# Optimization experiments

Hardware: AMD Instinct MI355X
Metric: run time of the kernel (lower is better)

## Reference

```python
import jax, jax.numpy as jnp
import numpy as np
import math

EMBED_DIM = 2048
NUM_HEADS = 32
GROUPS = 4
HEAD_DIM = EMBED_DIM // NUM_HEADS  # 64
HPG = NUM_HEADS // GROUPS          # heads per group = 8


def setup_inputs() -> dict:
    key = jax.random.key(0)
    k_x, k_wq, k_bq, k_wkv, k_bkv = jax.random.split(key, 5)
    B, L = 4, 4096
    scale = 1.0 / math.sqrt(EMBED_DIM)
    return {
        "x": jax.random.normal(k_x, (B, L, EMBED_DIM), dtype=jnp.float32),
        "Wq": jax.random.normal(k_wq, (EMBED_DIM, EMBED_DIM), dtype=jnp.float32) * scale,
        "bq": jax.random.normal(k_bq, (EMBED_DIM,), dtype=jnp.float32) * 0.01,
        "Wkv": jax.random.normal(k_wkv, (EMBED_DIM, 2 * HEAD_DIM * GROUPS), dtype=jnp.float32) * scale,
        "bkv": jax.random.normal(k_bkv, (2 * HEAD_DIM * GROUPS,), dtype=jnp.float32) * 0.01,
    }


def reference(x, Wq, bq, Wkv, bkv):
    B, L, _ = x.shape
    # projections
    q = (x @ Wq + bq).reshape(B, L, GROUPS, HPG, HEAD_DIM)          # blghd
    kv = (x @ Wkv + bkv).reshape(B, L, GROUPS, 2, HEAD_DIM)
    k, v = kv[:, :, :, 0], kv[:, :, :, 1]                            # blgd
    # scores: q @ k^T with k of shape (..., 1, head_dim) -> (..., HPG, 1)
    scores = jnp.einsum("blghd,blgd->blgh", q, k)[..., None] / math.sqrt(HEAD_DIM)
    attn = jax.nn.softmax(scores, axis=-1)                           # size-1 axis -> ones
    # attn @ v: (..., HPG, 1) @ (..., 1, head_dim) -> (..., HPG, head_dim)
    out = attn * v[:, :, :, None, :]                                 # blghd
    return out.reshape(B, L, EMBED_DIM)
```

## Files before the change

kernel.cpp:

```cpp
#include <hip/hip_runtime.h>


#define EMBED 2048
#define SV 272

typedef _Float16 half8 __attribute__((ext_vector_type(8)));
typedef _Float16 half4v __attribute__((ext_vector_type(4)));
typedef float f32x4 __attribute__((ext_vector_type(4)));

#define GLOAD16(g, l)                                                      \
  __builtin_amdgcn_global_load_lds(                                        \
      (const __attribute__((address_space(1))) void*)(g),                  \
      (__attribute__((address_space(3))) void*)(l), 16, 0, 0)

__global__ __launch_bounds__(256) void prep_b(const float* __restrict__ Wkv,
                                              _Float16* __restrict__ Bt) {
  const int t = threadIdx.x;
  const int kb = blockIdx.x * 4;
  const int vcol = ((t >> 6) * 128) + 64 + (t & 63);
  float v[4];
#pragma unroll
  for (int i = 0; i < 4; ++i) v[i] = Wkv[(size_t)(kb + i) * 512 + vcol];
  half4v h;
#pragma unroll
  for (int i = 0; i < 4; ++i) h[i] = (_Float16)v[i];
  *(half4v*)&Bt[(size_t)t * EMBED + kb] = h;
}

__global__ __launch_bounds__(256) void gqa_main(
    const float* __restrict__ x, const _Float16* __restrict__ Bt,
    const float* __restrict__ bkv, float* __restrict__ out) {
  __shared__ __align__(16) char smem[3 * 16384 + 3 * 32768];
  char* const Ab = smem;
  char* const Bb = smem + 3 * 16384;
  float* const Vs = (float*)smem;

  const int tid = threadIdx.x;
  const int w = tid >> 6;
  const int lane = tid & 63;
  const int lm = lane & 15;
  const int lq = lane >> 4;
  const int row0 = blockIdx.x * 64;

  const int acol = ((lane & 7) ^ (lane >> 3)) << 4;
  const char* asrc = (const char*)x +
      (size_t)(row0 + w * 16 + (lane >> 3)) * (EMBED * 4) + acol;
  const int adst0 = (w * 16) * 128;
  const int bcol = (((lane & 3) ^ ((lane >> 3) & 3)) << 4);
  const char* bsrc = (const char*)Bt +
      (size_t)(w * 64 + (lane >> 2)) * (EMBED * 2) + bcol;
  const int bdst0 = (w * 64) * 64;

#define STAGE(b, s)                                                        \
  {                                                                        \
    const char* as_ = asrc + (size_t)(s) * 256;                            \
    char* ad_ = Ab + (b) * 16384 + adst0;                                  \
    GLOAD16(as_, ad_);                                                     \
    GLOAD16(as_ + (size_t)8 * EMBED * 4, ad_ + 1024);                      \
    GLOAD16(as_ + 128, ad_ + 8192);                                        \
    GLOAD16(as_ + (size_t)8 * EMBED * 4 + 128, ad_ + 8192 + 1024);         \
    const char* bs_ = bsrc + (size_t)(s) * 128;                            \
    char* bd_ = Bb + (b) * 32768 + bdst0;                                  \
    GLOAD16(bs_, bd_);                                                     \
    GLOAD16(bs_ + (size_t)16 * EMBED * 2, bd_ + 1024);                     \
    GLOAD16(bs_ + (size_t)32 * EMBED * 2, bd_ + 2048);                     \
    GLOAD16(bs_ + (size_t)48 * EMBED * 2, bd_ + 3072);                     \
    GLOAD16(bs_ + 64, bd_ + 16384);                                        \
    GLOAD16(bs_ + (size_t)16 * EMBED * 2 + 64, bd_ + 16384 + 1024);        \
    GLOAD16(bs_ + (size_t)32 * EMBED * 2 + 64, bd_ + 16384 + 2048);        \
    GLOAD16(bs_ + (size_t)48 * EMBED * 2 + 64, bd_ + 16384 + 3072);        \
  }

  const int arswz = (lm & 7) << 4;
  const int brswz = ((lm >> 1) & 3) << 4;

#define LOADFRAG(b, roa, rob)                                              \
  {                                                                        \
    const char* Ar_ = Ab + (b) * 16384 + (roa) + lm * 128;                 \
    const char* Br_ = Bb + (b) * 32768 + (rob) + (w * 64 + lm) * 64 +      \
                      ((lq << 4) ^ brswz);                                 \
    _Pragma("unroll") for (int ni = 0; ni < 4; ++ni)                       \
        bfr_[ni] = *(const half8*)(Br_ + ni * 1024);                       \
    _Pragma("unroll") for (int mi = 0; mi < 4; ++mi) {                     \
      a0r_[mi] = *(const f32x4*)(Ar_ + mi * 2048 + ((lq << 5) ^ arswz));   \
      a1r_[mi] =                                                           \
          *(const f32x4*)(Ar_ + mi * 2048 + (((lq << 5) + 16) ^ arswz));   \
    }                                                                      \
  }
#define MFMAFRAG()                                                         \
  _Pragma("unroll") for (int mi = 0; mi < 4; ++mi) {                       \
    half8 af_;                                                             \
    _Pragma("unroll") for (int j = 0; j < 4; ++j)                          \
        af_[j] = (_Float16)a0r_[mi][j];                                    \
    _Pragma("unroll") for (int j = 0; j < 4; ++j)                          \
        af_[4 + j] = (_Float16)a1r_[mi][j];                                \
    _Pragma("unroll") for (int ni = 0; ni < 4; ++ni)                       \
        acc[mi][ni] = __builtin_amdgcn_mfma_f32_16x16x32_f16(              \
            af_, bfr_[ni], acc[mi][ni], 0, 0, 0);                          \
  }

  f32x4 acc[4][4] = {};

  STAGE(0, 0);
  STAGE(1, 1);

#define ITER(T, BC, BS)                                                    \
  {                                                                        \
    asm volatile("s_waitcnt vmcnt(12)" ::: "memory");                      \
    __builtin_amdgcn_s_barrier();                                          \
    f32x4 a0r_[4], a1r_[4];                                                \
    half8 bfr_[4];                                                         \
    LOADFRAG(BC, 0, 0);                                                    \
    {                                                                      \
      const int ss_ = (T) + 2 < 32 ? (T) + 2 : 31;                         \
      STAGE(BS, ss_);                                                      \
    }                                                                      \
    MFMAFRAG();                                                            \
    LOADFRAG(BC, 8192, 16384);                                             \
    MFMAFRAG();                                                            \
  }

  for (int tt = 0; tt < 30; tt += 3) {
    ITER(tt + 0, 0, 2)
    ITER(tt + 1, 1, 0)
    ITER(tt + 2, 2, 1)
  }
  ITER(30, 0, 2)
  ITER(31, 1, 0)
#undef ITER

  asm volatile("s_waitcnt vmcnt(0)" ::: "memory");
  __syncthreads();

  float bias[4];
#pragma unroll
  for (int ni = 0; ni < 4; ++ni) bias[ni] = bkv[w * 128 + 64 + ni * 16 + lm];

#pragma unroll
  for (int c = 0; c < 8; ++c) {
    const int mi = c >> 1;
    if ((lq >> 1) == (c & 1)) {
#pragma unroll
      for (int ni = 0; ni < 4; ++ni) {
        const int n = w * 64 + ni * 16 + lm;
        f32x4 v = acc[mi][ni];
#pragma unroll
        for (int r = 0; r < 4; ++r)
          Vs[((lq & 1) * 4 + r) * SV + n] = v[r] + bias[ni];
      }
    }
    __syncthreads();
    f32x4* out4 = (f32x4*)(out + (size_t)(row0 + c * 8) * EMBED);
#pragma unroll 4
    for (int i = 0; i < 16; ++i) {
      const int f = i * 256 + tid;
      const int row = f >> 9;
      const int c4 = f & 511;
      const int grp = c4 >> 7;
      const int d4 = c4 & 15;
      out4[(size_t)row * 512 + c4] =
          *(const f32x4*)&Vs[row * SV + grp * 64 + d4 * 4];
    }
    __syncthreads();
  }
}

extern "C" void kernel_launch(void* const* d_in, const int* in_sizes, int n_in,
                              void* d_out, int out_size, void* d_ws, size_t ws_size,
                              hipStream_t stream) {
  const float* x = (const float*)d_in[0];
  const float* Wkv = (const float*)d_in[3];
  const float* bkv = (const float*)d_in[4];
  float* out = (float*)d_out;
  _Float16* Bt = (_Float16*)d_ws;

  prep_b<<<512, 256, 0, stream>>>(Wkv, Bt);
  gqa_main<<<256, 256, 0, stream>>>(x, Bt, bkv, out);
}
```

Baseline: 262.3 us.

## Restructure GEMM pipeline with wide A stripes and finer B slabs

Splits staging of the fp32 activation tile and the fp16 weight tile into separate schedules. A is loaded in 128-wide K stripes (512 bytes per row) into two double-buffered buffers with a new XOR swizzle, while B is loaded in 32-wide K slabs through a four-deep ring. Each barrier step now issues one MFMA fragment instead of two. The goal is longer contiguous global reads for x and deeper prefetch of B. In exchange it adds more barriers per K and uses a different LDS footprint with hand-tuned vmcnt waits that must match the issue order.

```diff
diff --git a/kernel.cpp b/kernel.cpp
--- a/kernel.cpp
+++ b/kernel.cpp
@@ -30,9 +30,9 @@
 __global__ __launch_bounds__(256) void gqa_main(
     const float* __restrict__ x, const _Float16* __restrict__ Bt,
     const float* __restrict__ bkv, float* __restrict__ out) {
-  __shared__ __align__(16) char smem[3 * 16384 + 3 * 32768];
+  __shared__ __align__(16) char smem[2 * 32768 + 4 * 16384];
   char* const Ab = smem;
-  char* const Bb = smem + 3 * 16384;
+  char* const Bb = smem + 2 * 32768;
   float* const Vs = (float*)smem;
 
   const int tid = threadIdx.x;
@@ -40,51 +40,55 @@
   const int lane = tid & 63;
   const int lm = lane & 15;
   const int lq = lane >> 4;
+  const int lm7 = lm & 7;
   const int row0 = blockIdx.x * 64;
 
-  const int acol = ((lane & 7) ^ (lane >> 3)) << 4;
-  const char* asrc = (const char*)x +
-      (size_t)(row0 + w * 16 + (lane >> 3)) * (EMBED * 4) + acol;
-  const int adst0 = (w * 16) * 128;
+  const int arl = lane >> 5;
+  const int aslot16 = (lane & 31) * 16;
+  const char* axrowp =
+      (const char*)x + (size_t)(row0 + w * 16 + arl) * (EMBED * 4);
+  const int awdst = w * 8192;
+
+#define ASTAGE(ba, sidx)                                                   \
+  {                                                                        \
+    const size_t so_ = (size_t)(sidx) * 512;                               \
+    _Pragma("unroll") for (int i_ = 0; i_ < 8; ++i_) {                     \
+      GLOAD16(axrowp + (size_t)i_ * 2 * (EMBED * 4) + so_ +                \
+                  (aslot16 ^ ((((i_ * 2) + arl) & 7) << 4)),               \
+              Ab + (ba) * 32768 + awdst + i_ * 1024);                      \
+    }                                                                      \
+  }
+
   const int bcol = (((lane & 3) ^ ((lane >> 3) & 3)) << 4);
   const char* bsrc = (const char*)Bt +
       (size_t)(w * 64 + (lane >> 2)) * (EMBED * 2) + bcol;
   const int bdst0 = (w * 64) * 64;
 
-#define STAGE(b, s)                                                        \
+#define BSTAGE(bb, t)                                                      \
   {                                                                        \
-    const char* as_ = asrc + (size_t)(s) * 256;                            \
-    char* ad_ = Ab + (b) * 16384 + adst0;                                  \
-    GLOAD16(as_, ad_);                                                     \
-    GLOAD16(as_ + (size_t)8 * EMBED * 4, ad_ + 1024);                      \
-    GLOAD16(as_ + 128, ad_ + 8192);                                        \
-    GLOAD16(as_ + (size_t)8 * EMBED * 4 + 128, ad_ + 8192 + 1024);         \
-    const char* bs_ = bsrc + (size_t)(s) * 128;                            \
-    char* bd_ = Bb + (b) * 32768 + bdst0;                                  \
+    const char* bs_ = bsrc + (size_t)(t) * 64;                             \
+    char* bd_ = Bb + (bb) * 16384 + bdst0;                                 \
     GLOAD16(bs_, bd_);                                                     \
     GLOAD16(bs_ + (size_t)16 * EMBED * 2, bd_ + 1024);                     \
     GLOAD16(bs_ + (size_t)32 * EMBED * 2, bd_ + 2048);                     \
     GLOAD16(bs_ + (size_t)48 * EMBED * 2, bd_ + 3072);                     \
-    GLOAD16(bs_ + 64, bd_ + 16384);                                        \
-    GLOAD16(bs_ + (size_t)16 * EMBED * 2 + 64, bd_ + 16384 + 1024);        \
-    GLOAD16(bs_ + (size_t)32 * EMBED * 2 + 64, bd_ + 16384 + 2048);        \
-    GLOAD16(bs_ + (size_t)48 * EMBED * 2 + 64, bd_ + 16384 + 3072);        \
   }
 
-  const int arswz = (lm & 7) << 4;
+  const char* ard = Ab + lm * 512;
+  const int alq0 = ((lq * 2) ^ lm7) << 4;
+  const int alq1 = ((lq * 2 + 1) ^ lm7) << 4;
   const int brswz = ((lm >> 1) & 3) << 4;
+  const char* brd = Bb + (w * 64 + lm) * 64 + ((lq << 4) ^ brswz);
 
-#define LOADFRAG(b, roa, rob)                                              \
+#define LOADFRAG(BA, BB, J)                                                \
   {                                                                        \
-    const char* Ar_ = Ab + (b) * 16384 + (roa) + lm * 128;                 \
-    const char* Br_ = Bb + (b) * 32768 + (rob) + (w * 64 + lm) * 64 +      \
-                      ((lq << 4) ^ brswz);                                 \
     _Pragma("unroll") for (int ni = 0; ni < 4; ++ni)                       \
-        bfr_[ni] = *(const half8*)(Br_ + ni * 1024);                       \
+        bfr_[ni] = *(const half8*)(brd + (BB) * 16384 + ni * 1024);        \
     _Pragma("unroll") for (int mi = 0; mi < 4; ++mi) {                     \
-      a0r_[mi] = *(const f32x4*)(Ar_ + mi * 2048 + ((lq << 5) ^ arswz));   \
+      a0r_[mi] =                                                           \
+          *(const f32x4*)(ard + (BA) * 32768 + mi * 8192 + (J) * 128 + alq0); \
       a1r_[mi] =                                                           \
-          *(const f32x4*)(Ar_ + mi * 2048 + (((lq << 5) + 16) ^ arswz));   \
+          *(const f32x4*)(ard + (BA) * 32768 + mi * 8192 + (J) * 128 + alq1); \
     }                                                                      \
   }
 #define MFMAFRAG()                                                         \
@@ -101,33 +105,40 @@
 
   f32x4 acc[4][4] = {};
 
-  STAGE(0, 0);
-  STAGE(1, 1);
+  ASTAGE(0, 0);
+  BSTAGE(0, 0);
+  BSTAGE(1, 1);
+  BSTAGE(2, 2);
 
-#define ITER(T, BC, BS)                                                    \
+#define SLAB(BA, BN, S, J, BBUF, BSTG, WAITM)                              \
   {                                                                        \
-    asm volatile("s_waitcnt vmcnt(12)" ::: "memory");                      \
+    asm volatile("s_waitcnt vmcnt(" WAITM ")" ::: "memory");               \
     __builtin_amdgcn_s_barrier();                                          \
     f32x4 a0r_[4], a1r_[4];                                                \
     half8 bfr_[4];                                                         \
-    LOADFRAG(BC, 0, 0);                                                    \
+    LOADFRAG(BA, BBUF, J);                                                 \
+    if ((J) == 0) {                                                        \
+      const int sn_ = (S) + 1 < 16 ? (S) + 1 : 15;                         \
+      ASTAGE(BN, sn_);                                                     \
+    }                                                                      \
     {                                                                      \
-      const int ss_ = (T) + 2 < 32 ? (T) + 2 : 31;                         \
-      STAGE(BS, ss_);                                                      \
+      const int bt_ = 4 * (S) + 3 + (J);                                   \
+      BSTAGE(BSTG, bt_ < 64 ? bt_ : 63);                                   \
     }                                                                      \
     MFMAFRAG();                                                            \
-    LOADFRAG(BC, 8192, 16384);                                             \
-    MFMAFRAG();                                                            \
   }
+#define STRIPE(S, BA, BN)                                                  \
+  SLAB(BA, BN, S, 0, 0, 3, "8")                                            \
+  SLAB(BA, BN, S, 1, 1, 0, "16")                                           \
+  SLAB(BA, BN, S, 2, 2, 1, "16")                                           \
+  SLAB(BA, BN, S, 3, 3, 2, "8")
 
-  for (int tt = 0; tt < 30; tt += 3) {
-    ITER(tt + 0, 0, 2)
-    ITER(tt + 1, 1, 0)
-    ITER(tt + 2, 2, 1)
+  for (int ss = 0; ss < 16; ss += 2) {
+    STRIPE(ss, 0, 1)
+    STRIPE(ss + 1, 1, 0)
   }
-  ITER(30, 0, 2)
-  ITER(31, 1, 0)
-#undef ITER
+#undef STRIPE
+#undef SLAB
 
   asm volatile("s_waitcnt vmcnt(0)" ::: "memory");
   __syncthreads();
```

Measured after the change: 266.0 us. Within noise of the previous version (+1.4%).

## Use 8 waves per block with 2x4 warp tiling and 4-stage K=32 pipeline

Applied to the files above, without the earlier changes.

Doubles the block to 512 threads and splits the 64x256 output tile 2 ways in M and 4 ways in N, so each wave holds half as many accumulators. The K step is halved to 32 and the LDS ring grows from 3 to 4 smaller stages, keeping three loads in flight. The goal is more waves per CU to hide the latency of the memory-bound x stream. In exchange there are twice as many barriers per K, and each wave reloads B fragments for fewer MFMAs.

```diff
diff --git a/kernel.cpp b/kernel.cpp
--- a/kernel.cpp
+++ b/kernel.cpp
@@ -27,68 +27,59 @@
   *(half4v*)&Bt[(size_t)t * EMBED + kb] = h;
 }
 
-__global__ __launch_bounds__(256) void gqa_main(
+__global__ __launch_bounds__(512, 2) void gqa_main(
     const float* __restrict__ x, const _Float16* __restrict__ Bt,
     const float* __restrict__ bkv, float* __restrict__ out) {
-  __shared__ __align__(16) char smem[3 * 16384 + 3 * 32768];
+  __shared__ __align__(16) char smem[4 * 8192 + 4 * 16384];
   char* const Ab = smem;
-  char* const Bb = smem + 3 * 16384;
+  char* const Bb = smem + 4 * 8192;
   float* const Vs = (float*)smem;
 
   const int tid = threadIdx.x;
-  const int w = tid >> 6;
+  const int v = tid >> 6;
   const int lane = tid & 63;
   const int lm = lane & 15;
   const int lq = lane >> 4;
+  const int wm = v & 1;
+  const int wn = v >> 1;
   const int row0 = blockIdx.x * 64;
 
   const int acol = ((lane & 7) ^ (lane >> 3)) << 4;
   const char* asrc = (const char*)x +
-      (size_t)(row0 + w * 16 + (lane >> 3)) * (EMBED * 4) + acol;
-  const int adst0 = (w * 16) * 128;
+      (size_t)(row0 + v * 8 + (lane >> 3)) * (EMBED * 4) + acol;
+  const int adst = v * 1024;
   const int bcol = (((lane & 3) ^ ((lane >> 3) & 3)) << 4);
   const char* bsrc = (const char*)Bt +
-      (size_t)(w * 64 + (lane >> 2)) * (EMBED * 2) + bcol;
-  const int bdst0 = (w * 64) * 64;
+      (size_t)(v * 16 + (lane >> 2)) * (EMBED * 2) + bcol;
+  const int bdst = v * 1024;
 
 #define STAGE(b, s)                                                        \
   {                                                                        \
-    const char* as_ = asrc + (size_t)(s) * 256;                            \
-    char* ad_ = Ab + (b) * 16384 + adst0;                                  \
-    GLOAD16(as_, ad_);                                                     \
-    GLOAD16(as_ + (size_t)8 * EMBED * 4, ad_ + 1024);                      \
-    GLOAD16(as_ + 128, ad_ + 8192);                                        \
-    GLOAD16(as_ + (size_t)8 * EMBED * 4 + 128, ad_ + 8192 + 1024);         \
-    const char* bs_ = bsrc + (size_t)(s) * 128;                            \
-    char* bd_ = Bb + (b) * 32768 + bdst0;                                  \
-    GLOAD16(bs_, bd_);                                                     \
-    GLOAD16(bs_ + (size_t)16 * EMBED * 2, bd_ + 1024);                     \
-    GLOAD16(bs_ + (size_t)32 * EMBED * 2, bd_ + 2048);                     \
-    GLOAD16(bs_ + (size_t)48 * EMBED * 2, bd_ + 3072);                     \
-    GLOAD16(bs_ + 64, bd_ + 16384);                                        \
-    GLOAD16(bs_ + (size_t)16 * EMBED * 2 + 64, bd_ + 16384 + 1024);        \
-    GLOAD16(bs_ + (size_t)32 * EMBED * 2 + 64, bd_ + 16384 + 2048);        \
-    GLOAD16(bs_ + (size_t)48 * EMBED * 2 + 64, bd_ + 16384 + 3072);        \
+    GLOAD16(asrc + (size_t)(s) * 128, Ab + (b) * 8192 + adst);             \
+    const char* bs_ = bsrc + (size_t)(s) * 64;                             \
+    GLOAD16(bs_, Bb + (b) * 16384 + bdst);                                 \
+    GLOAD16(bs_ + (size_t)128 * EMBED * 2,                                 \
+            Bb + (b) * 16384 + 8192 + bdst);                               \
   }
 
   const int arswz = (lm & 7) << 4;
   const int brswz = ((lm >> 1) & 3) << 4;
+  const char* ard = Ab + (wm * 32 + lm) * 128;
+  const char* brd = Bb + (wn * 64 + lm) * 64 + ((lq << 4) ^ brswz);
 
-#define LOADFRAG(b, roa, rob)                                              \
+#define LOADFRAG(BC)                                                       \
   {                                                                        \
-    const char* Ar_ = Ab + (b) * 16384 + (roa) + lm * 128;                 \
-    const char* Br_ = Bb + (b) * 32768 + (rob) + (w * 64 + lm) * 64 +      \
-                      ((lq << 4) ^ brswz);                                 \
     _Pragma("unroll") for (int ni = 0; ni < 4; ++ni)                       \
-        bfr_[ni] = *(const half8*)(Br_ + ni * 1024);                       \
-    _Pragma("unroll") for (int mi = 0; mi < 4; ++mi) {                     \
-      a0r_[mi] = *(const f32x4*)(Ar_ + mi * 2048 + ((lq << 5) ^ arswz));   \
-      a1r_[mi] =                                                           \
-          *(const f32x4*)(Ar_ + mi * 2048 + (((lq << 5) + 16) ^ arswz));   \
+        bfr_[ni] = *(const half8*)(brd + (BC) * 16384 + ni * 1024);        \
+    _Pragma("unroll") for (int mi = 0; mi < 2; ++mi) {                     \
+      a0r_[mi] =                                                           \
+          *(const f32x4*)(ard + (BC) * 8192 + mi * 2048 + ((lq << 5) ^ arswz)); \
+      a1r_[mi] = *(const f32x4*)(ard + (BC) * 8192 + mi * 2048 +           \
+                                 (((lq << 5) + 16) ^ arswz));              \
     }                                                                      \
   }
 #define MFMAFRAG()                                                         \
-  _Pragma("unroll") for (int mi = 0; mi < 4; ++mi) {                       \
+  _Pragma("unroll") for (int mi = 0; mi < 2; ++mi) {                       \
     half8 af_;                                                             \
     _Pragma("unroll") for (int j = 0; j < 4; ++j)                          \
         af_[j] = (_Float16)a0r_[mi][j];                                    \
@@ -99,61 +90,58 @@
             af_, bfr_[ni], acc[mi][ni], 0, 0, 0);                          \
   }
 
-  f32x4 acc[4][4] = {};
+  f32x4 acc[2][4] = {};
 
   STAGE(0, 0);
   STAGE(1, 1);
+  STAGE(2, 2);
 
+  for (int tt = 0; tt < 64; tt += 4) {
 #define ITER(T, BC, BS)                                                    \
-  {                                                                        \
-    asm volatile("s_waitcnt vmcnt(12)" ::: "memory");                      \
-    __builtin_amdgcn_s_barrier();                                          \
-    f32x4 a0r_[4], a1r_[4];                                                \
-    half8 bfr_[4];                                                         \
-    LOADFRAG(BC, 0, 0);                                                    \
     {                                                                      \
-      const int ss_ = (T) + 2 < 32 ? (T) + 2 : 31;                         \
-      STAGE(BS, ss_);                                                      \
-    }                                                                      \
-    MFMAFRAG();                                                            \
-    LOADFRAG(BC, 8192, 16384);                                             \
-    MFMAFRAG();                                                            \
-  }
-
-  for (int tt = 0; tt < 30; tt += 3) {
-    ITER(tt + 0, 0, 2)
+      asm volatile("s_waitcnt vmcnt(6)" ::: "memory");                     \
+      __builtin_amdgcn_s_barrier();                                        \
+      f32x4 a0r_[2], a1r_[2];                                              \
+      half8 bfr_[4];                                                       \
+      LOADFRAG(BC);                                                        \
+      {                                                                    \
+        const int ss_ = (T) + 3 < 64 ? (T) + 3 : 63;                       \
+        STAGE(BS, ss_);                                                    \
+      }                                                                    \
+      MFMAFRAG();                                                          \
+    }
+    ITER(tt + 0, 0, 3)
     ITER(tt + 1, 1, 0)
     ITER(tt + 2, 2, 1)
+    ITER(tt + 3, 3, 2)
+#undef ITER
   }
-  ITER(30, 0, 2)
-  ITER(31, 1, 0)
-#undef ITER
 
   asm volatile("s_waitcnt vmcnt(0)" ::: "memory");
   __syncthreads();
 
   float bias[4];
 #pragma unroll
-  for (int ni = 0; ni < 4; ++ni) bias[ni] = bkv[w * 128 + 64 + ni * 16 + lm];
+  for (int ni = 0; ni < 4; ++ni) bias[ni] = bkv[wn * 128 + 64 + ni * 16 + lm];
 
 #pragma unroll
   for (int c = 0; c < 8; ++c) {
-    const int mi = c >> 1;
-    if ((lq >> 1) == (c & 1)) {
+    const int mi = (c >> 1) & 1;
+    if (wm == (c >> 2) && (lq >> 1) == (c & 1)) {
 #pragma unroll
       for (int ni = 0; ni < 4; ++ni) {
-        const int n = w * 64 + ni * 16 + lm;
-        f32x4 v = acc[mi][ni];
+        const int n = wn * 64 + ni * 16 + lm;
+        f32x4 vv = acc[mi][ni];
 #pragma unroll
         for (int r = 0; r < 4; ++r)
-          Vs[((lq & 1) * 4 + r) * SV + n] = v[r] + bias[ni];
+          Vs[((lq & 1) * 4 + r) * SV + n] = vv[r] + bias[ni];
       }
     }
     __syncthreads();
     f32x4* out4 = (f32x4*)(out + (size_t)(row0 + c * 8) * EMBED);
-#pragma unroll 4
-    for (int i = 0; i < 16; ++i) {
-      const int f = i * 256 + tid;
+#pragma unroll
+    for (int i = 0; i < 8; ++i) {
+      const int f = i * 512 + tid;
       const int row = f >> 9;
       const int c4 = f & 511;
       const int grp = c4 >> 7;
@@ -175,5 +163,5 @@
   _Float16* Bt = (_Float16*)d_ws;
 
   prep_b<<<512, 256, 0, stream>>>(Wkv, Bt);
-  gqa_main<<<256, 256, 0, stream>>>(x, Bt, bkv, out);
+  gqa_main<<<256, 512, 0, stream>>>(x, Bt, bkv, out);
 }
```

After: 268.9 us. +2.5%, slower.
